# Kernel optimization log

Hardware: AMD Instinct MI355X
Metric: run time of the kernel (lower is better)

## Reference

```python
import jax, jax.numpy as jnp
import numpy as np

N_NODES = 100000
N_EDGES = 1600000
IN_DIM = 48
HID = 16
N_CLASSES = 8


def _sage_conv(x, src, dst, W_l, W_r, b, n_nodes):
    # PyG SAGEConv (aggr='mean', root_weight=True):
    #   out_i = W_l @ mean_{j in N(i)} x_j + b + W_r @ x_i
    msg = x[src]                                              # [E, F]
    agg = jax.ops.segment_sum(msg, dst, num_segments=n_nodes)  # [N, F]
    deg = jax.ops.segment_sum(jnp.ones((src.shape[0],), x.dtype), dst,
                              num_segments=n_nodes)            # [N]
    agg = agg / jnp.maximum(deg, 1.0)[:, None]
    return agg @ W_l.T + b + x @ W_r.T


def setup_inputs() -> dict:
    key = jax.random.key(0)
    ks = jax.random.split(key, 10)
    def lin(k, out_d, in_d):
        s = 1.0 / np.sqrt(in_d)
        return jax.random.uniform(k, (out_d, in_d), jnp.float32, -s, s)
    x = jax.random.normal(ks[0], (N_NODES, IN_DIM), jnp.float32)
    edge_index = jax.random.randint(ks[1], (2, N_EDGES), 0, N_NODES, jnp.int64)
    return {
        "x": x,
        "edge_index": edge_index,
        "W1_l": lin(ks[2], HID, IN_DIM), "W1_r": lin(ks[3], HID, IN_DIM),
        "b1": jnp.zeros((HID,), jnp.float32),
        "W2_l": lin(ks[4], HID, HID), "W2_r": lin(ks[5], HID, HID),
        "b2": jnp.zeros((HID,), jnp.float32),
        "W3_l": lin(ks[6], N_CLASSES, HID), "W3_r": lin(ks[7], N_CLASSES, HID),
        "b3": jnp.zeros((N_CLASSES,), jnp.float32),
    }


def reference(x, edge_index, W1_l, W1_r, b1, W2_l, W2_r, b2, W3_l, W3_r, b3):
    src, dst = edge_index[0], edge_index[1]
    n = x.shape[0]
    # dropout is identity in deterministic/eval reference
    h = jax.nn.elu(_sage_conv(x, src, dst, W1_l, W1_r, b1, n))
    h = jax.nn.elu(_sage_conv(h, src, dst, W2_l, W2_r, b2, n))
    h = jax.nn.elu(_sage_conv(h, src, dst, W3_l, W3_r, b3, n))
    return jax.nn.log_softmax(h, axis=-1)
```

## Files before the change

### kernel.cpp

```cpp
#include <hip/hip_runtime.h>
#include <hip/hip_bf16.h>
#include <math.h>

#define N_IN   48
#define N_HID  16
#define N_CLS  8
#define CAP    48
#define NB_SHIFT 9
#define TILE   4096
#define CAPB   9216
#define WSTR   52

__device__ __forceinline__ float bf2f(unsigned short u) {
    union { unsigned int i; float f; } c;
    c.i = ((unsigned int)u) << 16;
    return c.f;
}
__device__ __forceinline__ unsigned short f2bf(float f) {
    unsigned int u = __float_as_uint(f);
    unsigned int r = u + 0x7FFFu + ((u >> 16) & 1u);
    return (unsigned short)(r >> 16);
}

__global__ __launch_bounds__(256) void scatter_tiles_kernel(
        const int* __restrict__ src, const int* __restrict__ dst,
        int* __restrict__ cursor, int* __restrict__ ebuf, int E) {
    __shared__ int lh[256];
    __shared__ int gbase[256];
    __shared__ int rank[256];
    int t = threadIdx.x;
    lh[t] = 0;
    rank[t] = 0;
    __syncthreads();
    int base = blockIdx.x * TILE;
    int dcache[TILE / 256];
#pragma unroll
    for (int k = 0; k < TILE / 256; k++) {
        int e = base + t + k * 256;
        dcache[k] = -1;
        if (e < E) {
            int d = dst[e];
            dcache[k] = d;
            atomicAdd(&lh[d >> NB_SHIFT], 1);
        }
    }
    __syncthreads();
    if (lh[t]) gbase[t] = atomicAdd(&cursor[t], lh[t]);
    __syncthreads();
#pragma unroll
    for (int k = 0; k < TILE / 256; k++) {
        int e = base + t + k * 256;
        if (e < E) {
            int d = dcache[k];
            int b = d >> NB_SHIFT;
            int r = gbase[b] + atomicAdd(&rank[b], 1);
            if (r < CAPB)
                ebuf[b * CAPB + r] = ((d & 511) << 17) | src[e];
        }
    }
}

__global__ __launch_bounds__(256) void fill_proj_kernel(
        const int* __restrict__ cursor, const int* __restrict__ ebuf,
        int* __restrict__ cnt, int* __restrict__ adj,
        const float* __restrict__ X,
        const float* __restrict__ Wl, const float* __restrict__ Wr,
        const float* __restrict__ b,
        unsigned short* __restrict__ P, unsigned short* __restrict__ S,
        int N, int nbuck) {
    __shared__ int   lc[512];
    __shared__ float sWl[N_HID * WSTR];
    __shared__ float sWr[N_HID * WSTR];
    __shared__ float sb[N_HID];
    int t = threadIdx.x;

    if ((int)blockIdx.x < nbuck) {
        int bb = blockIdx.x;
        int nodeBeg = bb << NB_SHIFT;
        for (int i = t; i < 512; i += 256) lc[i] = 0;
        __syncthreads();
        int nb = cursor[bb];
        if (nb > CAPB) nb = CAPB;
        int beg = bb * CAPB, end = beg + nb;
        for (int e = beg + t; e < end; e += 256) {
            int v = ebuf[e];
            int ld = ((unsigned int)v) >> 17;
            int s  = v & 0x1FFFF;
            int p = atomicAdd(&lc[ld], 1);
            if (p < CAP) adj[(size_t)(nodeBeg + ld) * CAP + p] = s;
        }
        __syncthreads();
        for (int i = t; nodeBeg + i < N && i < 512; i += 256)
            cnt[nodeBeg + i] = lc[i];
        return;
    }

    for (int idx = t; idx < N_HID * N_IN; idx += 256) {
        int r = idx / N_IN, k = idx - r * N_IN;
        sWl[r * WSTR + k] = Wl[idx];
        sWr[r * WSTR + k] = Wr[idx];
    }
    if (t < N_HID) sb[t] = b[t];
    __syncthreads();

    int node = ((int)blockIdx.x - nbuck) * 64 + (t >> 2);
    int q = t & 3;
    if (node >= N) return;

    const float4* xrow = reinterpret_cast<const float4*>(X + (size_t)node * N_IN);
    float accL[4], accR[4];
#pragma unroll
    for (int oo = 0; oo < 4; oo++) { accL[oo] = 0.0f; accR[oo] = sb[4 * q + oo]; }

#pragma unroll
    for (int c = 0; c < N_IN / 4; c++) {
        float4 xv = xrow[c];
#pragma unroll
        for (int oo = 0; oo < 4; oo++) {
            int row = 4 * q + oo;
            float4 wl = *reinterpret_cast<const float4*>(&sWl[row * WSTR + 4 * c]);
            float4 wr = *reinterpret_cast<const float4*>(&sWr[row * WSTR + 4 * c]);
            accL[oo] = fmaf(xv.x, wl.x, accL[oo]); accR[oo] = fmaf(xv.x, wr.x, accR[oo]);
            accL[oo] = fmaf(xv.y, wl.y, accL[oo]); accR[oo] = fmaf(xv.y, wr.y, accR[oo]);
            accL[oo] = fmaf(xv.z, wl.z, accL[oo]); accR[oo] = fmaf(xv.z, wr.z, accR[oo]);
            accL[oo] = fmaf(xv.w, wl.w, accL[oo]); accR[oo] = fmaf(xv.w, wr.w, accR[oo]);
        }
    }

    int gid = node * 4 + q;
    reinterpret_cast<ushort4*>(P)[gid] =
        make_ushort4(f2bf(accL[0]), f2bf(accL[1]), f2bf(accL[2]), f2bf(accL[3]));
    reinterpret_cast<ushort4*>(S)[gid] =
        make_ushort4(f2bf(accR[0]), f2bf(accR[1]), f2bf(accR[2]), f2bf(accR[3]));
}

__global__ __launch_bounds__(256) void gather_proj16_kernel(
        const int* __restrict__ cnt, const int* __restrict__ adj,
        const unsigned short* __restrict__ Pin, const unsigned short* __restrict__ Sin,
        const float* __restrict__ Wl, const float* __restrict__ Wr,
        const float* __restrict__ bias,
        unsigned short* __restrict__ Pout, unsigned short* __restrict__ Sout, int N) {
    int gid = blockIdx.x * blockDim.x + threadIdx.x;
    if (gid >= N * 4) return;
    int i = gid >> 2;
    int q = gid & 3;
    int deg = cnt[i];
    if (deg > CAP) deg = CAP;
    const int* lst = adj + (size_t)i * CAP;
    ushort4 svu = reinterpret_cast<const ushort4*>(Sin)[gid];
    float4 acc = make_float4(0.f, 0.f, 0.f, 0.f);
    const ushort4* P4 = reinterpret_cast<const ushort4*>(Pin);
    int e = 0;
    for (; e + 8 <= deg; e += 8) {
        int4 ja = *reinterpret_cast<const int4*>(lst + e);
        int4 jb = *reinterpret_cast<const int4*>(lst + e + 4);
        ushort4 t0 = P4[(size_t)ja.x * 4 + q];
        ushort4 t1 = P4[(size_t)ja.y * 4 + q];
        ushort4 t2 = P4[(size_t)ja.z * 4 + q];
        ushort4 t3 = P4[(size_t)ja.w * 4 + q];
        ushort4 t4 = P4[(size_t)jb.x * 4 + q];
        ushort4 t5 = P4[(size_t)jb.y * 4 + q];
        ushort4 t6 = P4[(size_t)jb.z * 4 + q];
        ushort4 t7 = P4[(size_t)jb.w * 4 + q];
        acc.x += ((bf2f(t0.x) + bf2f(t1.x)) + (bf2f(t2.x) + bf2f(t3.x)))
               + ((bf2f(t4.x) + bf2f(t5.x)) + (bf2f(t6.x) + bf2f(t7.x)));
        acc.y += ((bf2f(t0.y) + bf2f(t1.y)) + (bf2f(t2.y) + bf2f(t3.y)))
               + ((bf2f(t4.y) + bf2f(t5.y)) + (bf2f(t6.y) + bf2f(t7.y)));
        acc.z += ((bf2f(t0.z) + bf2f(t1.z)) + (bf2f(t2.z) + bf2f(t3.z)))
               + ((bf2f(t4.z) + bf2f(t5.z)) + (bf2f(t6.z) + bf2f(t7.z)));
        acc.w += ((bf2f(t0.w) + bf2f(t1.w)) + (bf2f(t2.w) + bf2f(t3.w)))
               + ((bf2f(t4.w) + bf2f(t5.w)) + (bf2f(t6.w) + bf2f(t7.w)));
    }
    for (; e + 4 <= deg; e += 4) {
        int4 js = *reinterpret_cast<const int4*>(lst + e);
        ushort4 t0 = P4[(size_t)js.x * 4 + q];
        ushort4 t1 = P4[(size_t)js.y * 4 + q];
        ushort4 t2 = P4[(size_t)js.z * 4 + q];
        ushort4 t3 = P4[(size_t)js.w * 4 + q];
        acc.x += (bf2f(t0.x) + bf2f(t1.x)) + (bf2f(t2.x) + bf2f(t3.x));
        acc.y += (bf2f(t0.y) + bf2f(t1.y)) + (bf2f(t2.y) + bf2f(t3.y));
        acc.z += (bf2f(t0.z) + bf2f(t1.z)) + (bf2f(t2.z) + bf2f(t3.z));
        acc.w += (bf2f(t0.w) + bf2f(t1.w)) + (bf2f(t2.w) + bf2f(t3.w));
    }
    for (; e < deg; e++) {
        ushort4 t = P4[(size_t)lst[e] * 4 + q];
        acc.x += bf2f(t.x); acc.y += bf2f(t.y);
        acc.z += bf2f(t.z); acc.w += bf2f(t.w);
    }
    float inv = 1.0f / (float)max(deg, 1);
    float4 h;
    h.x = acc.x * inv + bf2f(svu.x); h.y = acc.y * inv + bf2f(svu.y);
    h.z = acc.z * inv + bf2f(svu.z); h.w = acc.w * inv + bf2f(svu.w);
    h.x = h.x > 0.f ? h.x : expm1f(h.x);
    h.y = h.y > 0.f ? h.y : expm1f(h.y);
    h.z = h.z > 0.f ? h.z : expm1f(h.z);
    h.w = h.w > 0.f ? h.w : expm1f(h.w);

    int lane = threadIdx.x & 63;
    int lb = lane & ~3;
    float hv[16];
#pragma unroll
    for (int a = 0; a < 4; a++) {
        hv[4 * a + 0] = __shfl(h.x, lb + a, 64);
        hv[4 * a + 1] = __shfl(h.y, lb + a, 64);
        hv[4 * a + 2] = __shfl(h.z, lb + a, 64);
        hv[4 * a + 3] = __shfl(h.w, lb + a, 64);
    }

    const float4* Wl4 = reinterpret_cast<const float4*>(Wl);
    const float4* Wr4 = reinterpret_cast<const float4*>(Wr);
    float pl[4], sr[4];
#pragma unroll
    for (int oo = 0; oo < 4; oo++) {
        int o = 4 * q + oo;
        float aL = 0.0f, aR = bias[o];
#pragma unroll
        for (int c = 0; c < 4; c++) {
            float4 wl = Wl4[o * 4 + c];
            float4 wr = Wr4[o * 4 + c];
            aL = fmaf(hv[4 * c + 0], wl.x, aL); aR = fmaf(hv[4 * c + 0], wr.x, aR);
            aL = fmaf(hv[4 * c + 1], wl.y, aL); aR = fmaf(hv[4 * c + 1], wr.y, aR);
            aL = fmaf(hv[4 * c + 2], wl.z, aL); aR = fmaf(hv[4 * c + 2], wr.z, aR);
            aL = fmaf(hv[4 * c + 3], wl.w, aL); aR = fmaf(hv[4 * c + 3], wr.w, aR);
        }
        pl[oo] = aL; sr[oo] = aR;
    }
    reinterpret_cast<ushort4*>(Pout)[gid] =
        make_ushort4(f2bf(pl[0]), f2bf(pl[1]), f2bf(pl[2]), f2bf(pl[3]));
    reinterpret_cast<ushort4*>(Sout)[gid] =
        make_ushort4(f2bf(sr[0]), f2bf(sr[1]), f2bf(sr[2]), f2bf(sr[3]));
}

__global__ __launch_bounds__(256) void gather_proj8_kernel(
        const int* __restrict__ cnt, const int* __restrict__ adj,
        const unsigned short* __restrict__ Pin, const unsigned short* __restrict__ Sin,
        const float* __restrict__ Wl, const float* __restrict__ Wr,
        const float* __restrict__ bias,
        unsigned int* __restrict__ Pout, unsigned int* __restrict__ Sout, int N) {
    int gid = blockIdx.x * blockDim.x + threadIdx.x;
    if (gid >= N * 4) return;
    int i = gid >> 2;
    int q = gid & 3;
    int deg = cnt[i];
    if (deg > CAP) deg = CAP;
    const int* lst = adj + (size_t)i * CAP;
    ushort4 svu = reinterpret_cast<const ushort4*>(Sin)[gid];
    float4 acc = make_float4(0.f, 0.f, 0.f, 0.f);
    const ushort4* P4 = reinterpret_cast<const ushort4*>(Pin);
    int e = 0;
    for (; e + 8 <= deg; e += 8) {
        int4 ja = *reinterpret_cast<const int4*>(lst + e);
        int4 jb = *reinterpret_cast<const int4*>(lst + e + 4);
        ushort4 t0 = P4[(size_t)ja.x * 4 + q];
        ushort4 t1 = P4[(size_t)ja.y * 4 + q];
        ushort4 t2 = P4[(size_t)ja.z * 4 + q];
        ushort4 t3 = P4[(size_t)ja.w * 4 + q];
        ushort4 t4 = P4[(size_t)jb.x * 4 + q];
        ushort4 t5 = P4[(size_t)jb.y * 4 + q];
        ushort4 t6 = P4[(size_t)jb.z * 4 + q];
        ushort4 t7 = P4[(size_t)jb.w * 4 + q];
        acc.x += ((bf2f(t0.x) + bf2f(t1.x)) + (bf2f(t2.x) + bf2f(t3.x)))
               + ((bf2f(t4.x) + bf2f(t5.x)) + (bf2f(t6.x) + bf2f(t7.x)));
        acc.y += ((bf2f(t0.y) + bf2f(t1.y)) + (bf2f(t2.y) + bf2f(t3.y)))
               + ((bf2f(t4.y) + bf2f(t5.y)) + (bf2f(t6.y) + bf2f(t7.y)));
        acc.z += ((bf2f(t0.z) + bf2f(t1.z)) + (bf2f(t2.z) + bf2f(t3.z)))
               + ((bf2f(t4.z) + bf2f(t5.z)) + (bf2f(t6.z) + bf2f(t7.z)));
        acc.w += ((bf2f(t0.w) + bf2f(t1.w)) + (bf2f(t2.w) + bf2f(t3.w)))
               + ((bf2f(t4.w) + bf2f(t5.w)) + (bf2f(t6.w) + bf2f(t7.w)));
    }
    for (; e + 4 <= deg; e += 4) {
        int4 js = *reinterpret_cast<const int4*>(lst + e);
        ushort4 t0 = P4[(size_t)js.x * 4 + q];
        ushort4 t1 = P4[(size_t)js.y * 4 + q];
        ushort4 t2 = P4[(size_t)js.z * 4 + q];
        ushort4 t3 = P4[(size_t)js.w * 4 + q];
        acc.x += (bf2f(t0.x) + bf2f(t1.x)) + (bf2f(t2.x) + bf2f(t3.x));
        acc.y += (bf2f(t0.y) + bf2f(t1.y)) + (bf2f(t2.y) + bf2f(t3.y));
        acc.z += (bf2f(t0.z) + bf2f(t1.z)) + (bf2f(t2.z) + bf2f(t3.z));
        acc.w += (bf2f(t0.w) + bf2f(t1.w)) + (bf2f(t2.w) + bf2f(t3.w));
    }
    for (; e < deg; e++) {
        ushort4 t = P4[(size_t)lst[e] * 4 + q];
        acc.x += bf2f(t.x); acc.y += bf2f(t.y);
        acc.z += bf2f(t.z); acc.w += bf2f(t.w);
    }
    float inv = 1.0f / (float)max(deg, 1);
    float4 h;
    h.x = acc.x * inv + bf2f(svu.x); h.y = acc.y * inv + bf2f(svu.y);
    h.z = acc.z * inv + bf2f(svu.z); h.w = acc.w * inv + bf2f(svu.w);
    h.x = h.x > 0.f ? h.x : expm1f(h.x);
    h.y = h.y > 0.f ? h.y : expm1f(h.y);
    h.z = h.z > 0.f ? h.z : expm1f(h.z);
    h.w = h.w > 0.f ? h.w : expm1f(h.w);

    int lane = threadIdx.x & 63;
    int lb = lane & ~3;
    float hv[16];
#pragma unroll
    for (int a = 0; a < 4; a++) {
        hv[4 * a + 0] = __shfl(h.x, lb + a, 64);
        hv[4 * a + 1] = __shfl(h.y, lb + a, 64);
        hv[4 * a + 2] = __shfl(h.z, lb + a, 64);
        hv[4 * a + 3] = __shfl(h.w, lb + a, 64);
    }

    const float4* Wl4 = reinterpret_cast<const float4*>(Wl);
    const float4* Wr4 = reinterpret_cast<const float4*>(Wr);
    float pl[2], sr[2];
#pragma unroll
    for (int oo = 0; oo < 2; oo++) {
        int o = 2 * q + oo;
        float aL = 0.0f, aR = bias[o];
#pragma unroll
        for (int c = 0; c < 4; c++) {
            float4 wl = Wl4[o * 4 + c];
            float4 wr = Wr4[o * 4 + c];
            aL = fmaf(hv[4 * c + 0], wl.x, aL); aR = fmaf(hv[4 * c + 0], wr.x, aR);
            aL = fmaf(hv[4 * c + 1], wl.y, aL); aR = fmaf(hv[4 * c + 1], wr.y, aR);
            aL = fmaf(hv[4 * c + 2], wl.z, aL); aR = fmaf(hv[4 * c + 2], wr.z, aR);
            aL = fmaf(hv[4 * c + 3], wl.w, aL); aR = fmaf(hv[4 * c + 3], wr.w, aR);
        }
        pl[oo] = aL; sr[oo] = aR;
    }
    Pout[gid] = ((unsigned int)f2bf(pl[1]) << 16) | f2bf(pl[0]);
    Sout[gid] = ((unsigned int)f2bf(sr[1]) << 16) | f2bf(sr[0]);
}

__global__ __launch_bounds__(256) void gather8_kernel(
        const int* __restrict__ cnt, const int* __restrict__ adj,
        const unsigned short* __restrict__ P, const unsigned short* __restrict__ S,
        float* __restrict__ out, int N) {
    int gid = blockIdx.x * blockDim.x + threadIdx.x;
    if (gid >= N * 2) return;
    int i = gid >> 1;
    int q = gid & 1;
    int deg = cnt[i];
    if (deg > CAP) deg = CAP;
    const int* lst = adj + (size_t)i * CAP;
    ushort4 svu = reinterpret_cast<const ushort4*>(S)[gid];
    float4 acc = make_float4(0.f, 0.f, 0.f, 0.f);
    const ushort4* P4 = reinterpret_cast<const ushort4*>(P);
    int e = 0;
    for (; e + 8 <= deg; e += 8) {
        int4 ja = *reinterpret_cast<const int4*>(lst + e);
        int4 jb = *reinterpret_cast<const int4*>(lst + e + 4);
        ushort4 t0 = P4[(size_t)ja.x * 2 + q];
        ushort4 t1 = P4[(size_t)ja.y * 2 + q];
        ushort4 t2 = P4[(size_t)ja.z * 2 + q];
        ushort4 t3 = P4[(size_t)ja.w * 2 + q];
        ushort4 t4 = P4[(size_t)jb.x * 2 + q];
        ushort4 t5 = P4[(size_t)jb.y * 2 + q];
        ushort4 t6 = P4[(size_t)jb.z * 2 + q];
        ushort4 t7 = P4[(size_t)jb.w * 2 + q];
        acc.x += ((bf2f(t0.x) + bf2f(t1.x)) + (bf2f(t2.x) + bf2f(t3.x)))
               + ((bf2f(t4.x) + bf2f(t5.x)) + (bf2f(t6.x) + bf2f(t7.x)));
        acc.y += ((bf2f(t0.y) + bf2f(t1.y)) + (bf2f(t2.y) + bf2f(t3.y)))
               + ((bf2f(t4.y) + bf2f(t5.y)) + (bf2f(t6.y) + bf2f(t7.y)));
        acc.z += ((bf2f(t0.z) + bf2f(t1.z)) + (bf2f(t2.z) + bf2f(t3.z)))
               + ((bf2f(t4.z) + bf2f(t5.z)) + (bf2f(t6.z) + bf2f(t7.z)));
        acc.w += ((bf2f(t0.w) + bf2f(t1.w)) + (bf2f(t2.w) + bf2f(t3.w)))
               + ((bf2f(t4.w) + bf2f(t5.w)) + (bf2f(t6.w) + bf2f(t7.w)));
    }
    for (; e + 4 <= deg; e += 4) {
        int4 js = *reinterpret_cast<const int4*>(lst + e);
        ushort4 t0 = P4[(size_t)js.x * 2 + q];
        ushort4 t1 = P4[(size_t)js.y * 2 + q];
        ushort4 t2 = P4[(size_t)js.z * 2 + q];
        ushort4 t3 = P4[(size_t)js.w * 2 + q];
        acc.x += (bf2f(t0.x) + bf2f(t1.x)) + (bf2f(t2.x) + bf2f(t3.x));
        acc.y += (bf2f(t0.y) + bf2f(t1.y)) + (bf2f(t2.y) + bf2f(t3.y));
        acc.z += (bf2f(t0.z) + bf2f(t1.z)) + (bf2f(t2.z) + bf2f(t3.z));
        acc.w += (bf2f(t0.w) + bf2f(t1.w)) + (bf2f(t2.w) + bf2f(t3.w));
    }
    for (; e < deg; e++) {
        ushort4 t = P4[(size_t)lst[e] * 2 + q];
        acc.x += bf2f(t.x); acc.y += bf2f(t.y);
        acc.z += bf2f(t.z); acc.w += bf2f(t.w);
    }
    float inv = 1.0f / (float)max(deg, 1);
    float4 v;
    v.x = acc.x * inv + bf2f(svu.x); v.y = acc.y * inv + bf2f(svu.y);
    v.z = acc.z * inv + bf2f(svu.z); v.w = acc.w * inv + bf2f(svu.w);
    v.x = v.x > 0.f ? v.x : expm1f(v.x);
    v.y = v.y > 0.f ? v.y : expm1f(v.y);
    v.z = v.z > 0.f ? v.z : expm1f(v.z);
    v.w = v.w > 0.f ? v.w : expm1f(v.w);
    float m = fmaxf(fmaxf(v.x, v.y), fmaxf(v.z, v.w));
    m = fmaxf(m, __shfl_xor(m, 1));
    float sum = expf(v.x - m) + expf(v.y - m) + expf(v.z - m) + expf(v.w - m);
    sum += __shfl_xor(sum, 1);
    float lse = m + logf(sum);
    reinterpret_cast<float4*>(out)[gid] =
        make_float4(v.x - lse, v.y - lse, v.z - lse, v.w - lse);
}

extern "C" void kernel_launch(void* const* d_in, const int* in_sizes, int n_in,
                              void* d_out, int out_size, void* d_ws, size_t ws_size,
                              hipStream_t stream) {
    const float* x   = (const float*)d_in[0];
    const int*   ei  = (const int*)d_in[1];
    const float* W1l = (const float*)d_in[2];
    const float* W1r = (const float*)d_in[3];
    const float* b1  = (const float*)d_in[4];
    const float* W2l = (const float*)d_in[5];
    const float* W2r = (const float*)d_in[6];
    const float* b2  = (const float*)d_in[7];
    const float* W3l = (const float*)d_in[8];
    const float* W3r = (const float*)d_in[9];
    const float* b3  = (const float*)d_in[10];
    float* out = (float*)d_out;

    const int N = in_sizes[0] / N_IN;
    const int E = in_sizes[1] / 2;
    const int* src = ei;
    const int* dst = ei + E;
    const int nbuck = (N + 511) >> NB_SHIFT;

    int* cursor = (int*)d_ws;
    int* cnt    = cursor + 256;
    int  Npad   = (N + 3) & ~3;
    int* adj    = cnt + Npad;
    int* ebuf   = adj + (size_t)N * CAP;
    unsigned short* P1 = (unsigned short*)(ebuf + (size_t)nbuck * CAPB);
    unsigned short* P2 = P1 + (size_t)N * N_HID;
    unsigned short* S1 = P2 + (size_t)N * N_HID;
    unsigned short* S3 = S1 + (size_t)N * N_HID;
    unsigned short* P3 = P1;

    hipMemsetAsync(cursor, 0, 256 * sizeof(int), stream);

    const int B = 256;
    int n4Grid   = (N * 4 + B - 1) / B;
    int n2Grid   = (N * 2 + B - 1) / B;
    int p1Grid   = (N + 63) / 64;
    int tileGrid = (E + TILE - 1) / TILE;

    scatter_tiles_kernel<<<tileGrid, B, 0, stream>>>(src, dst, cursor, ebuf, E);

    fill_proj_kernel<<<nbuck + p1Grid, B, 0, stream>>>(
        cursor, ebuf, cnt, adj, x, W1l, W1r, b1, P1, S1, N, nbuck);

    gather_proj16_kernel<<<n4Grid, B, 0, stream>>>(cnt, adj, P1, S1,
                                                   W2l, W2r, b2, P2, S1, N);

    gather_proj8_kernel<<<n4Grid, B, 0, stream>>>(cnt, adj, P2, S1,
                                                  W3l, W3r, b3,
                                                  (unsigned int*)P3,
                                                  (unsigned int*)S3, N);

    gather8_kernel<<<n2Grid, B, 0, stream>>>(cnt, adj, P3, S3, out, N);
}
```

Before: 217.3 us.

## Pad adjacency lists to multiples of 16 with a zero sentinel node for branch-light gathers

The fill stage now pads each node's neighbour list up to a multiple of 16 with the index N, and every projection stage writes a zero row for that sentinel node. The three gather kernels load the first 32 neighbour indices as int4 vectors up front and accumulate in fixed chunks of 16 through a shared helper, replacing the variable-length 8/4/1 loops. The aim is more independent loads in flight and less per-lane loop divergence and tail handling. In exchange, lanes issue redundant loads of the sentinel row, the fill stage does extra padding stores, and every intermediate buffer grows by one row.

```diff
diff --git a/kernel.cpp b/kernel.cpp
--- a/kernel.cpp
+++ b/kernel.cpp
@@ -20,6 +20,42 @@
     unsigned int u = __float_as_uint(f);
     unsigned int r = u + 0x7FFFu + ((u >> 16) & 1u);
     return (unsigned short)(r >> 16);
+}
+
+__device__ __forceinline__ void acc16(const ushort4* __restrict__ P4, int mul, int q,
+        int4 a0, int4 a1, int4 a2, int4 a3, float4& acc) {
+    ushort4 t0 = P4[(size_t)a0.x * mul + q];
+    ushort4 t1 = P4[(size_t)a0.y * mul + q];
+    ushort4 t2 = P4[(size_t)a0.z * mul + q];
+    ushort4 t3 = P4[(size_t)a0.w * mul + q];
+    ushort4 t4 = P4[(size_t)a1.x * mul + q];
+    ushort4 t5 = P4[(size_t)a1.y * mul + q];
+    ushort4 t6 = P4[(size_t)a1.z * mul + q];
+    ushort4 t7 = P4[(size_t)a1.w * mul + q];
+    ushort4 t8 = P4[(size_t)a2.x * mul + q];
+    ushort4 t9 = P4[(size_t)a2.y * mul + q];
+    ushort4 ta = P4[(size_t)a2.z * mul + q];
+    ushort4 tb = P4[(size_t)a2.w * mul + q];
+    ushort4 tc = P4[(size_t)a3.x * mul + q];
+    ushort4 td = P4[(size_t)a3.y * mul + q];
+    ushort4 te = P4[(size_t)a3.z * mul + q];
+    ushort4 tf = P4[(size_t)a3.w * mul + q];
+    acc.x += ((((bf2f(t0.x)+bf2f(t1.x))+(bf2f(t2.x)+bf2f(t3.x)))
+             + ((bf2f(t4.x)+bf2f(t5.x))+(bf2f(t6.x)+bf2f(t7.x))))
+            + (((bf2f(t8.x)+bf2f(t9.x))+(bf2f(ta.x)+bf2f(tb.x)))
+             + ((bf2f(tc.x)+bf2f(td.x))+(bf2f(te.x)+bf2f(tf.x)))));
+    acc.y += ((((bf2f(t0.y)+bf2f(t1.y))+(bf2f(t2.y)+bf2f(t3.y)))
+             + ((bf2f(t4.y)+bf2f(t5.y))+(bf2f(t6.y)+bf2f(t7.y))))
+            + (((bf2f(t8.y)+bf2f(t9.y))+(bf2f(ta.y)+bf2f(tb.y)))
+             + ((bf2f(tc.y)+bf2f(td.y))+(bf2f(te.y)+bf2f(tf.y)))));
+    acc.z += ((((bf2f(t0.z)+bf2f(t1.z))+(bf2f(t2.z)+bf2f(t3.z)))
+             + ((bf2f(t4.z)+bf2f(t5.z))+(bf2f(t6.z)+bf2f(t7.z))))
+            + (((bf2f(t8.z)+bf2f(t9.z))+(bf2f(ta.z)+bf2f(tb.z)))
+             + ((bf2f(tc.z)+bf2f(td.z))+(bf2f(te.z)+bf2f(tf.z)))));
+    acc.w += ((((bf2f(t0.w)+bf2f(t1.w))+(bf2f(t2.w)+bf2f(t3.w)))
+             + ((bf2f(t4.w)+bf2f(t5.w))+(bf2f(t6.w)+bf2f(t7.w))))
+            + (((bf2f(t8.w)+bf2f(t9.w))+(bf2f(ta.w)+bf2f(tb.w)))
+             + ((bf2f(tc.w)+bf2f(td.w))+(bf2f(te.w)+bf2f(tf.w)))));
 }
 
 __global__ __launch_bounds__(256) void scatter_tiles_kernel(
@@ -90,8 +126,17 @@
             if (p < CAP) adj[(size_t)(nodeBeg + ld) * CAP + p] = s;
         }
         __syncthreads();
-        for (int i = t; nodeBeg + i < N && i < 512; i += 256)
-            cnt[nodeBeg + i] = lc[i];
+        for (int i = t; i < 512; i += 256) {
+            int node = nodeBeg + i;
+            if (node >= N) continue;
+            int c = lc[i];
+            cnt[node] = c;
+            if (c > CAP) c = CAP;
+            int degp = (c + 15) & ~15;
+            if (degp < 16) degp = 16;
+            int* row = adj + (size_t)node * CAP;
+            for (int p = c; p < degp; p++) row[p] = N;
+        }
         return;
     }
 
@@ -105,7 +150,13 @@
 
     int node = ((int)blockIdx.x - nbuck) * 64 + (t >> 2);
     int q = t & 3;
-    if (node >= N) return;
+    if (node > N) return;
+    int gid = node * 4 + q;
+    if (node == N) {
+        reinterpret_cast<ushort4*>(P)[gid] = make_ushort4(0, 0, 0, 0);
+        reinterpret_cast<ushort4*>(S)[gid] = make_ushort4(0, 0, 0, 0);
+        return;
+    }
 
     const float4* xrow = reinterpret_cast<const float4*>(X + (size_t)node * N_IN);
     float accL[4], accR[4];
@@ -127,7 +178,6 @@
         }
     }
 
-    int gid = node * 4 + q;
     reinterpret_cast<ushort4*>(P)[gid] =
         make_ushort4(f2bf(accL[0]), f2bf(accL[1]), f2bf(accL[2]), f2bf(accL[3]));
     reinterpret_cast<ushort4*>(S)[gid] =
@@ -142,50 +192,25 @@
         unsigned short* __restrict__ Pout, unsigned short* __restrict__ Sout, int N) {
     int gid = blockIdx.x * blockDim.x + threadIdx.x;
     if (gid >= N * 4) return;
+    if (gid < 4)
+        reinterpret_cast<ushort4*>(Pout)[(size_t)N * 4 + gid] = make_ushort4(0, 0, 0, 0);
     int i = gid >> 2;
     int q = gid & 3;
     int deg = cnt[i];
     if (deg > CAP) deg = CAP;
-    const int* lst = adj + (size_t)i * CAP;
+    int degp = (deg + 15) & ~15;
+    if (degp < 16) degp = 16;
+    const int4* lst4 = reinterpret_cast<const int4*>(adj + (size_t)i * CAP);
+    int4 a0 = lst4[0], a1 = lst4[1], a2 = lst4[2], a3 = lst4[3];
+    int4 b0 = lst4[4], b1 = lst4[5], b2 = lst4[6], b3 = lst4[7];
     ushort4 svu = reinterpret_cast<const ushort4*>(Sin)[gid];
+    const ushort4* P4 = reinterpret_cast<const ushort4*>(Pin);
     float4 acc = make_float4(0.f, 0.f, 0.f, 0.f);
-    const ushort4* P4 = reinterpret_cast<const ushort4*>(Pin);
-    int e = 0;
-    for (; e + 8 <= deg; e += 8) {
-        int4 ja = *reinterpret_cast<const int4*>(lst + e);
-        int4 jb = *reinterpret_cast<const int4*>(lst + e + 4);
-        ushort4 t0 = P4[(size_t)ja.x * 4 + q];
-        ushort4 t1 = P4[(size_t)ja.y * 4 + q];
-        ushort4 t2 = P4[(size_t)ja.z * 4 + q];
-        ushort4 t3 = P4[(size_t)ja.w * 4 + q];
-        ushort4 t4 = P4[(size_t)jb.x * 4 + q];
-        ushort4 t5 = P4[(size_t)jb.y * 4 + q];
-        ushort4 t6 = P4[(size_t)jb.z * 4 + q];
-        ushort4 t7 = P4[(size_t)jb.w * 4 + q];
-        acc.x += ((bf2f(t0.x) + bf2f(t1.x)) + (bf2f(t2.x) + bf2f(t3.x)))
-               + ((bf2f(t4.x) + bf2f(t5.x)) + (bf2f(t6.x) + bf2f(t7.x)));
-        acc.y += ((bf2f(t0.y) + bf2f(t1.y)) + (bf2f(t2.y) + bf2f(t3.y)))
-               + ((bf2f(t4.y) + bf2f(t5.y)) + (bf2f(t6.y) + bf2f(t7.y)));
-        acc.z += ((bf2f(t0.z) + bf2f(t1.z)) + (bf2f(t2.z) + bf2f(t3.z)))
-               + ((bf2f(t4.z) + bf2f(t5.z)) + (bf2f(t6.z) + bf2f(t7.z)));
-        acc.w += ((bf2f(t0.w) + bf2f(t1.w)) + (bf2f(t2.w) + bf2f(t3.w)))
-               + ((bf2f(t4.w) + bf2f(t5.w)) + (bf2f(t6.w) + bf2f(t7.w)));
-    }
-    for (; e + 4 <= deg; e += 4) {
-        int4 js = *reinterpret_cast<const int4*>(lst + e);
-        ushort4 t0 = P4[(size_t)js.x * 4 + q];
-        ushort4 t1 = P4[(size_t)js.y * 4 + q];
-        ushort4 t2 = P4[(size_t)js.z * 4 + q];
-        ushort4 t3 = P4[(size_t)js.w * 4 + q];
-        acc.x += (bf2f(t0.x) + bf2f(t1.x)) + (bf2f(t2.x) + bf2f(t3.x));
-        acc.y += (bf2f(t0.y) + bf2f(t1.y)) + (bf2f(t2.y) + bf2f(t3.y));
-        acc.z += (bf2f(t0.z) + bf2f(t1.z)) + (bf2f(t2.z) + bf2f(t3.z));
-        acc.w += (bf2f(t0.w) + bf2f(t1.w)) + (bf2f(t2.w) + bf2f(t3.w));
-    }
-    for (; e < deg; e++) {
-        ushort4 t = P4[(size_t)lst[e] * 4 + q];
-        acc.x += bf2f(t.x); acc.y += bf2f(t.y);
-        acc.z += bf2f(t.z); acc.w += bf2f(t.w);
+    acc16(P4, 4, q, a0, a1, a2, a3, acc);
+    if (degp > 16) {
+        acc16(P4, 4, q, b0, b1, b2, b3, acc);
+        if (degp > 32)
+            acc16(P4, 4, q, lst4[8], lst4[9], lst4[10], lst4[11], acc);
     }
     float inv = 1.0f / (float)max(deg, 1);
     float4 h;
@@ -239,50 +264,25 @@
         unsigned int* __restrict__ Pout, unsigned int* __restrict__ Sout, int N) {
     int gid = blockIdx.x * blockDim.x + threadIdx.x;
     if (gid >= N * 4) return;
+    if (gid < 4)
+        Pout[(size_t)N * 4 + gid] = 0u;
     int i = gid >> 2;
     int q = gid & 3;
     int deg = cnt[i];
     if (deg > CAP) deg = CAP;
-    const int* lst = adj + (size_t)i * CAP;
+    int degp = (deg + 15) & ~15;
+    if (degp < 16) degp = 16;
+    const int4* lst4 = reinterpret_cast<const int4*>(adj + (size_t)i * CAP);
+    int4 a0 = lst4[0], a1 = lst4[1], a2 = lst4[2], a3 = lst4[3];
+    int4 b0 = lst4[4], b1 = lst4[5], b2 = lst4[6], b3 = lst4[7];
     ushort4 svu = reinterpret_cast<const ushort4*>(Sin)[gid];
+    const ushort4* P4 = reinterpret_cast<const ushort4*>(Pin);
     float4 acc = make_float4(0.f, 0.f, 0.f, 0.f);
-    const ushort4* P4 = reinterpret_cast<const ushort4*>(Pin);
-    int e = 0;
-    for (; e + 8 <= deg; e += 8) {
-        int4 ja = *reinterpret_cast<const int4*>(lst + e);
-        int4 jb = *reinterpret_cast<const int4*>(lst + e + 4);
-        ushort4 t0 = P4[(size_t)ja.x * 4 + q];
-        ushort4 t1 = P4[(size_t)ja.y * 4 + q];
-        ushort4 t2 = P4[(size_t)ja.z * 4 + q];
-        ushort4 t3 = P4[(size_t)ja.w * 4 + q];
-        ushort4 t4 = P4[(size_t)jb.x * 4 + q];
-        ushort4 t5 = P4[(size_t)jb.y * 4 + q];
-        ushort4 t6 = P4[(size_t)jb.z * 4 + q];
-        ushort4 t7 = P4[(size_t)jb.w * 4 + q];
-        acc.x += ((bf2f(t0.x) + bf2f(t1.x)) + (bf2f(t2.x) + bf2f(t3.x)))
-               + ((bf2f(t4.x) + bf2f(t5.x)) + (bf2f(t6.x) + bf2f(t7.x)));
-        acc.y += ((bf2f(t0.y) + bf2f(t1.y)) + (bf2f(t2.y) + bf2f(t3.y)))
-               + ((bf2f(t4.y) + bf2f(t5.y)) + (bf2f(t6.y) + bf2f(t7.y)));
-        acc.z += ((bf2f(t0.z) + bf2f(t1.z)) + (bf2f(t2.z) + bf2f(t3.z)))
-               + ((bf2f(t4.z) + bf2f(t5.z)) + (bf2f(t6.z) + bf2f(t7.z)));
-        acc.w += ((bf2f(t0.w) + bf2f(t1.w)) + (bf2f(t2.w) + bf2f(t3.w)))
-               + ((bf2f(t4.w) + bf2f(t5.w)) + (bf2f(t6.w) + bf2f(t7.w)));
-    }
-    for (; e + 4 <= deg; e += 4) {
-        int4 js = *reinterpret_cast<const int4*>(lst + e);
-        ushort4 t0 = P4[(size_t)js.x * 4 + q];
-        ushort4 t1 = P4[(size_t)js.y * 4 + q];
-        ushort4 t2 = P4[(size_t)js.z * 4 + q];
-        ushort4 t3 = P4[(size_t)js.w * 4 + q];
-        acc.x += (bf2f(t0.x) + bf2f(t1.x)) + (bf2f(t2.x) + bf2f(t3.x));
-        acc.y += (bf2f(t0.y) + bf2f(t1.y)) + (bf2f(t2.y) + bf2f(t3.y));
-        acc.z += (bf2f(t0.z) + bf2f(t1.z)) + (bf2f(t2.z) + bf2f(t3.z));
-        acc.w += (bf2f(t0.w) + bf2f(t1.w)) + (bf2f(t2.w) + bf2f(t3.w));
-    }
-    for (; e < deg; e++) {
-        ushort4 t = P4[(size_t)lst[e] * 4 + q];
-        acc.x += bf2f(t.x); acc.y += bf2f(t.y);
-        acc.z += bf2f(t.z); acc.w += bf2f(t.w);
+    acc16(P4, 4, q, a0, a1, a2, a3, acc);
+    if (degp > 16) {
+        acc16(P4, 4, q, b0, b1, b2, b3, acc);
+        if (degp > 32)
+            acc16(P4, 4, q, lst4[8], lst4[9], lst4[10], lst4[11], acc);
     }
     float inv = 1.0f / (float)max(deg, 1);
     float4 h;
@@ -336,46 +336,19 @@
     int q = gid & 1;
     int deg = cnt[i];
     if (deg > CAP) deg = CAP;
-    const int* lst = adj + (size_t)i * CAP;
+    int degp = (deg + 15) & ~15;
+    if (degp < 16) degp = 16;
+    const int4* lst4 = reinterpret_cast<const int4*>(adj + (size_t)i * CAP);
+    int4 a0 = lst4[0], a1 = lst4[1], a2 = lst4[2], a3 = lst4[3];
+    int4 b0 = lst4[4], b1 = lst4[5], b2 = lst4[6], b3 = lst4[7];
     ushort4 svu = reinterpret_cast<const ushort4*>(S)[gid];
+    const ushort4* P4 = reinterpret_cast<const ushort4*>(P);
     float4 acc = make_float4(0.f, 0.f, 0.f, 0.f);
-    const ushort4* P4 = reinterpret_cast<const ushort4*>(P);
-    int e = 0;
-    for (; e + 8 <= deg; e += 8) {
-        int4 ja = *reinterpret_cast<const int4*>(lst + e);
-        int4 jb = *reinterpret_cast<const int4*>(lst + e + 4);
-        ushort4 t0 = P4[(size_t)ja.x * 2 + q];
-        ushort4 t1 = P4[(size_t)ja.y * 2 + q];
-        ushort4 t2 = P4[(size_t)ja.z * 2 + q];
-        ushort4 t3 = P4[(size_t)ja.w * 2 + q];
-        ushort4 t4 = P4[(size_t)jb.x * 2 + q];
-        ushort4 t5 = P4[(size_t)jb.y * 2 + q];
-        ushort4 t6 = P4[(size_t)jb.z * 2 + q];
-        ushort4 t7 = P4[(size_t)jb.w * 2 + q];
-        acc.x += ((bf2f(t0.x) + bf2f(t1.x)) + (bf2f(t2.x) + bf2f(t3.x)))
-               + ((bf2f(t4.x) + bf2f(t5.x)) + (bf2f(t6.x) + bf2f(t7.x)));
-        acc.y += ((bf2f(t0.y) + bf2f(t1.y)) + (bf2f(t2.y) + bf2f(t3.y)))
-               + ((bf2f(t4.y) + bf2f(t5.y)) + (bf2f(t6.y) + bf2f(t7.y)));
-        acc.z += ((bf2f(t0.z) + bf2f(t1.z)) + (bf2f(t2.z) + bf2f(t3.z)))
-               + ((bf2f(t4.z) + bf2f(t5.z)) + (bf2f(t6.z) + bf2f(t7.z)));
-        acc.w += ((bf2f(t0.w) + bf2f(t1.w)) + (bf2f(t2.w) + bf2f(t3.w)))
-               + ((bf2f(t4.w) + bf2f(t5.w)) + (bf2f(t6.w) + bf2f(t7.w)));
-    }
-    for (; e + 4 <= deg; e += 4) {
-        int4 js = *reinterpret_cast<const int4*>(lst + e);
-        ushort4 t0 = P4[(size_t)js.x * 2 + q];
-        ushort4 t1 = P4[(size_t)js.y * 2 + q];
-        ushort4 t2 = P4[(size_t)js.z * 2 + q];
-        ushort4 t3 = P4[(size_t)js.w * 2 + q];
-        acc.x += (bf2f(t0.x) + bf2f(t1.x)) + (bf2f(t2.x) + bf2f(t3.x));
-        acc.y += (bf2f(t0.y) + bf2f(t1.y)) + (bf2f(t2.y) + bf2f(t3.y));
-        acc.z += (bf2f(t0.z) + bf2f(t1.z)) + (bf2f(t2.z) + bf2f(t3.z));
-        acc.w += (bf2f(t0.w) + bf2f(t1.w)) + (bf2f(t2.w) + bf2f(t3.w));
-    }
-    for (; e < deg; e++) {
-        ushort4 t = P4[(size_t)lst[e] * 2 + q];
-        acc.x += bf2f(t.x); acc.y += bf2f(t.y);
-        acc.z += bf2f(t.z); acc.w += bf2f(t.w);
+    acc16(P4, 2, q, a0, a1, a2, a3, acc);
+    if (degp > 16) {
+        acc16(P4, 2, q, b0, b1, b2, b3, acc);
+        if (degp > 32)
+            acc16(P4, 2, q, lst4[8], lst4[9], lst4[10], lst4[11], acc);
     }
     float inv = 1.0f / (float)max(deg, 1);
     float4 v;
@@ -421,10 +394,11 @@
     int  Npad   = (N + 3) & ~3;
     int* adj    = cnt + Npad;
     int* ebuf   = adj + (size_t)N * CAP;
+    const size_t Nr = (size_t)N + 1;
     unsigned short* P1 = (unsigned short*)(ebuf + (size_t)nbuck * CAPB);
-    unsigned short* P2 = P1 + (size_t)N * N_HID;
-    unsigned short* S1 = P2 + (size_t)N * N_HID;
-    unsigned short* S3 = S1 + (size_t)N * N_HID;
+    unsigned short* P2 = P1 + Nr * N_HID;
+    unsigned short* S1 = P2 + Nr * N_HID;
+    unsigned short* S3 = S1 + Nr * N_HID;
     unsigned short* P3 = P1;
 
     hipMemsetAsync(cursor, 0, 256 * sizeof(int), stream);
@@ -432,7 +406,7 @@
     const int B = 256;
     int n4Grid   = (N * 4 + B - 1) / B;
     int n2Grid   = (N * 2 + B - 1) / B;
-    int p1Grid   = (N + 63) / 64;
+    int p1Grid   = (N + 1 + 63) / 64;
     int tileGrid = (E + TILE - 1) / TILE;
 
     scatter_tiles_kernel<<<tileGrid, B, 0, stream>>>(src, dst, cursor, ebuf, E);
```

Result: faster. 213.0 us (-2.0%).
